# Optimization experiments

Measured on AMD Instinct MI355X. Metric: run time of the kernel, lower is better.

## Reference

```python
import jax, jax.numpy as jnp
from jax import lax
import numpy as np

T, B, D_IN, D_H = 1024, 128, 512, 1024
W_SCALE = 0.02  # keep exp(a) in a sane range, like default small Linear init


def setup_inputs() -> dict:
    key = jax.random.key(0)
    ks = jax.random.split(key, 7)
    return {
        "x": jax.random.normal(ks[0], (T, B, D_IN), dtype=jnp.float32),
        "initial_state": jax.random.normal(ks[1], (D_H,), dtype=jnp.float32),
        "u_W": jax.random.normal(ks[2], (D_H, D_IN), dtype=jnp.float32) * W_SCALE,
        "u_b": jax.random.normal(ks[3], (D_H,), dtype=jnp.float32) * W_SCALE,
        "g_W": jax.random.normal(ks[4], (D_H, D_IN + D_H), dtype=jnp.float32) * W_SCALE,
        "g_b": jax.random.normal(ks[5], (D_H,), dtype=jnp.float32) * W_SCALE,
        "a_W": jax.random.normal(ks[6], (D_H, D_IN + D_H), dtype=jnp.float32) * W_SCALE,
    }


def reference(x, initial_state, u_W, u_b, g_W, g_b, a_W):
    # x: [T, B, D_in]; returns (hts [T, B, D_h], ht [B, D_h])
    batch = x.shape[1]
    d_h = initial_state.shape[0]
    ht0 = jnp.tanh(jnp.broadcast_to(initial_state, (batch, d_h)))
    n0 = jnp.zeros((batch, d_h), dtype=x.dtype)
    d0 = jnp.zeros((batch, d_h), dtype=x.dtype)

    def step(carry, x_step):
        n, d, ht = carry
        x_merge = jnp.concatenate([x_step, ht], axis=1)  # [B, D_in + D_h]
        u = x_step @ u_W.T + u_b
        g = x_merge @ g_W.T + g_b
        a = x_merge @ a_W.T
        z = u * jnp.tanh(g)
        ea = jnp.exp(a)
        n = n + z * ea
        d = d + ea
        ht = jnp.tanh(n / d)
        return (n, d, ht), ht

    (_, _, ht), hts = lax.scan(step, (n0, d0, ht0), x)
    return hts, ht
```

## Files before the change

### kernel.cpp

```cpp
#include <hip/hip_runtime.h>
#include <math.h>

#define T_STEPS 1024
#define NB 128
#define D_IN 512
#define D_H 1024
#define K_TOT 1536
#define N_A 3072
#define N_H 2048

typedef __bf16 bf16x8 __attribute__((ext_vector_type(8)));
typedef float f32x4 __attribute__((ext_vector_type(4)));
typedef unsigned long long u64;

__device__ __forceinline__ unsigned short f2bf(float f) {
    unsigned int u = __float_as_uint(f);
    unsigned int r = 0x7fffu + ((u >> 16) & 1u);
    return (unsigned short)((u + r) >> 16);
}
__device__ __forceinline__ float bf2f(unsigned short v) {
    return __uint_as_float(((unsigned int)v) << 16);
}
__device__ __forceinline__ float fast_tanh(float x) {
    float ax = fabsf(x);
    float e = __expf(2.0f * ax);
    float t = 1.0f - 2.0f / (e + 1.0f);
    return copysignf(t, x);
}


__global__ __launch_bounds__(256) void pack_wa(
    const float* __restrict__ uW, const float* __restrict__ gW,
    const float* __restrict__ aW, unsigned short* __restrict__ wa) {
    int i = blockIdx.x * 256 + threadIdx.x;
    if (i >= N_A * D_IN) return;
    int rr = i >> 9, k = i & 511;
    float v;
    if (rr < 1024)       v = uW[(size_t)rr * D_IN + k];
    else if (rr < 2048)  v = gW[(size_t)(rr - 1024) * K_TOT + k];
    else                 v = aW[(size_t)(rr - 2048) * K_TOT + k];
    wa[i] = f2bf(v);
}

__global__ __launch_bounds__(256) void pack_wh(
    const float* __restrict__ gW, const float* __restrict__ aW,
    unsigned short* __restrict__ wh) {
    int i = blockIdx.x * 256 + threadIdx.x;
    if (i >= N_H * D_H) return;
    int rr = i >> 10, k = i & 1023;
    int g = rr >> 5, ii = rr & 31, j = g * 16 + (ii & 15);
    const float* src = (ii < 16) ? gW : aW;
    wh[i] = f2bf(src[(size_t)j * K_TOT + D_IN + k]);
}

__global__ __launch_bounds__(256) void rwa_init(
    const float* __restrict__ init_st, float* __restrict__ nbuf,
    float* __restrict__ dbuf, unsigned short* __restrict__ hbuf,
    int* __restrict__ flags) {
    int i = blockIdx.x * 256 + threadIdx.x;
    if (i >= NB * D_H) return;
    nbuf[i] = 0.f; dbuf[i] = 0.f;
    hbuf[i] = f2bf(tanhf(init_st[i & (D_H - 1)]));
    if (i < 256) flags[i] = 0;
}


__global__ __launch_bounds__(256) void phase_a(
    const float* __restrict__ x, const unsigned short* __restrict__ wa,
    const float* __restrict__ ub, const float* __restrict__ gb,
    unsigned short* __restrict__ pre)
{
    __shared__ unsigned short As[128][72];
    __shared__ unsigned short Bs[128][72];
    const int tid = threadIdx.x;
    const int bn = blockIdx.x;
    const int bm = blockIdx.y;
    const int wave = tid >> 6, lane = tid & 63;
    const int wm = wave >> 1, wn = wave & 1;
    const int lr = lane & 15, lk = lane >> 4;

    f32x4 acc[4][4] = {};

    for (int k0 = 0; k0 < D_IN; k0 += 64) {
        for (int i = tid; i < 128 * 16; i += 256) {
            int r = i >> 4, c4 = (i & 15) * 4;
            float4 v = *(const float4*)&x[(size_t)(bm * 128 + r) * D_IN + k0 + c4];
            unsigned short* d = &As[r][c4];
            d[0] = f2bf(v.x); d[1] = f2bf(v.y); d[2] = f2bf(v.z); d[3] = f2bf(v.w);
        }
        for (int i = tid; i < 128 * 8; i += 256) {
            int r = i >> 3, c8 = (i & 7) * 8;
            *(uint4*)&Bs[r][c8] =
                *(const uint4*)&wa[(size_t)(bn * 128 + r) * D_IN + k0 + c8];
        }
        __syncthreads();
        #pragma unroll
        for (int ks = 0; ks < 2; ++ks) {
            bf16x8 af[4], bfr[4];
            #pragma unroll
            for (int mf = 0; mf < 4; ++mf)
                af[mf] = *(const bf16x8*)&As[wm * 64 + mf * 16 + lr][ks * 32 + lk * 8];
            #pragma unroll
            for (int nf = 0; nf < 4; ++nf)
                bfr[nf] = *(const bf16x8*)&Bs[wn * 64 + nf * 16 + lr][ks * 32 + lk * 8];
            #pragma unroll
            for (int mf = 0; mf < 4; ++mf)
                #pragma unroll
                for (int nf = 0; nf < 4; ++nf)
                    acc[mf][nf] = __builtin_amdgcn_mfma_f32_16x16x32_bf16(
                        af[mf], bfr[nf], acc[mf][nf], 0, 0, 0);
        }
        __syncthreads();
    }

    #pragma unroll
    for (int nf = 0; nf < 4; ++nf) {
        int n = bn * 128 + wn * 64 + nf * 16 + lr;
        float bias = (n < 1024) ? ub[n] : ((n < 2048) ? gb[n - 1024] : 0.f);
        #pragma unroll
        for (int mf = 0; mf < 4; ++mf) {
            int mbase = bm * 128 + wm * 64 + mf * 16 + lk * 4;
            #pragma unroll
            for (int r = 0; r < 4; ++r) {
                int mrow = mbase + r;
                pre[((size_t)(mrow >> 7) * N_A + n) * 128 + (mrow & 127)] =
                    f2bf(acc[mf][nf][r] + bias);
            }
        }
    }
}


__global__ __launch_bounds__(512) void rwa_persist(
    const unsigned short* __restrict__ wh,
    const unsigned short* __restrict__ pre,
    unsigned short* __restrict__ hbuf,
    float* __restrict__ nbuf, float* __restrict__ dbuf,
    float* __restrict__ out,
    int* __restrict__ flags,
    int t0, int nt)
{
    __shared__ unsigned short whs[32][1024];
    __shared__ unsigned short hs[32][1024];
    __shared__ float scr[6 * 512];

    const int tid = threadIdx.x;
    const int bid = blockIdx.x;
    const int bn = bid >> 2;
    const int bm = bid & 3;
    const int wave = tid >> 6, lane = tid & 63;
    const int wm = wave >> 2;
    const int kq = wave & 3;
    const int lr = lane & 15, lk = lane >> 4;

    for (int s = tid; s < 4096; s += 512) {
        int r = s >> 7, g = s & 127;
        uint4 v = *(const uint4*)&wh[(size_t)(bn * 32 + r) * 1024 + (size_t)g * 8];
        *(uint4*)&whs[r][(g ^ (r & 7)) * 8] = v;
    }

    const int j = bn * 16 + lr;
    const int bbase = bm * 32 + wm * 16 + lk * 4;
    float nr[4], dr[4];
    if (kq == 0) {
        #pragma unroll
        for (int r = 0; r < 4; ++r) {
            size_t idx = (size_t)(bbase + r) * D_H + j;
            nr[r] = nbuf[idx]; dr[r] = dbuf[idx];
        }
    }

    const int r0 = tid >> 7;
    const int gg = tid & 127;
    const unsigned short* hsrc0 =
        hbuf + (size_t)(bm * 32 + r0) * D_H + (size_t)gg * 8;
    const int* fp = flags + bm * 64 + lane;
    __syncthreads();

    for (int l = 0; l < nt; ++l) {
        const int t = t0 + l;

        u64 puL = 0, pgL = 0, paL = 0;
        if (kq == 0) {
            size_t pb = (size_t)l * N_A * 128;
            puL = *(const u64*)&pre[pb + ((size_t)j) * 128 + bbase];
            pgL = *(const u64*)&pre[pb + ((size_t)(1024 + j)) * 128 + bbase];
            paL = *(const u64*)&pre[pb + ((size_t)(2048 + j)) * 128 + bbase];
        }

        if (t > 0) {
            if (wave == 0) {
                for (;;) {
                    int v;
                    asm volatile("global_load_dword %0, %1, off sc0 sc1\n\t"
                                 "s_waitcnt vmcnt(0)"
                                 : "=v"(v) : "v"(fp) : "memory");
                    if (__all(v >= t)) break;
                    __builtin_amdgcn_s_sleep(1);
                }
            }
            __builtin_amdgcn_s_barrier();
        }

        {
            const unsigned short* hsrc = hsrc0 + (size_t)(t & 1) * NB * D_H;
            uint4 v0, v1, v2, v3, v4, v5, v6, v7;
            asm volatile("global_load_dwordx4 %0, %1, off sc0 sc1" : "=v"(v0) : "v"(hsrc)               : "memory");
            asm volatile("global_load_dwordx4 %0, %1, off sc0 sc1" : "=v"(v1) : "v"(hsrc + 4 * D_H)     : "memory");
            asm volatile("global_load_dwordx4 %0, %1, off sc0 sc1" : "=v"(v2) : "v"(hsrc + 8 * D_H)     : "memory");
            asm volatile("global_load_dwordx4 %0, %1, off sc0 sc1" : "=v"(v3) : "v"(hsrc + 12 * D_H)    : "memory");
            asm volatile("global_load_dwordx4 %0, %1, off sc0 sc1" : "=v"(v4) : "v"(hsrc + 16 * D_H)    : "memory");
            asm volatile("global_load_dwordx4 %0, %1, off sc0 sc1" : "=v"(v5) : "v"(hsrc + 20 * D_H)    : "memory");
            asm volatile("global_load_dwordx4 %0, %1, off sc0 sc1" : "=v"(v6) : "v"(hsrc + 24 * D_H)    : "memory");
            asm volatile("global_load_dwordx4 %0, %1, off sc0 sc1" : "=v"(v7) : "v"(hsrc + 28 * D_H)    : "memory");
            asm volatile("s_waitcnt vmcnt(0)" ::: "memory");
            *(uint4*)&hs[r0 +  0][(gg ^ r0) * 8]       = v0;
            *(uint4*)&hs[r0 +  4][(gg ^ r0 ^ 4) * 8]   = v1;
            *(uint4*)&hs[r0 +  8][(gg ^ r0) * 8]       = v2;
            *(uint4*)&hs[r0 + 12][(gg ^ r0 ^ 4) * 8]   = v3;
            *(uint4*)&hs[r0 + 16][(gg ^ r0) * 8]       = v4;
            *(uint4*)&hs[r0 + 20][(gg ^ r0 ^ 4) * 8]   = v5;
            *(uint4*)&hs[r0 + 24][(gg ^ r0) * 8]       = v6;
            *(uint4*)&hs[r0 + 28][(gg ^ r0 ^ 4) * 8]   = v7;
        }
        __syncthreads();

        f32x4 accg = {}, acca = {};
        const int ar = wm * 16 + lr;
        #pragma unroll
        for (int ks = 0; ks < 8; ++ks) {
            const int k = kq * 256 + ks * 32 + lk * 8;
            const int gidx = k >> 3;
            bf16x8 av = *(const bf16x8*)&hs[ar][(gidx ^ (ar & 7)) << 3];
            bf16x8 bg = *(const bf16x8*)&whs[lr][(gidx ^ (lr & 7)) << 3];
            bf16x8 ba = *(const bf16x8*)&whs[16 + lr][(gidx ^ (lr & 7)) << 3];
            accg = __builtin_amdgcn_mfma_f32_16x16x32_bf16(av, bg, accg, 0, 0, 0);
            acca = __builtin_amdgcn_mfma_f32_16x16x32_bf16(av, ba, acca, 0, 0, 0);
        }

        if (kq != 0) {
            int base = (wm * 3 + (kq - 1)) * 512 + lane * 4;
            *(f32x4*)&scr[base]       = accg;
            *(f32x4*)&scr[base + 256] = acca;
        }
        __syncthreads();

        if (kq == 0) {
            #pragma unroll
            for (int s = 0; s < 3; ++s) {
                int base = (wm * 3 + s) * 512 + lane * 4;
                accg += *(const f32x4*)&scr[base];
                acca += *(const f32x4*)&scr[base + 256];
            }
            unsigned short* hdst = hbuf + (size_t)((t + 1) & 1) * NB * D_H;
            float hv[4];
            #pragma unroll
            for (int r = 0; r < 4; ++r) {
                float u  = bf2f((unsigned short)(puL >> (16 * r)));
                float gx = bf2f((unsigned short)(pgL >> (16 * r)));
                float ax = bf2f((unsigned short)(paL >> (16 * r)));
                float g = gx + accg[r];
                float a = ax + acca[r];
                float ea = __expf(a);
                float z = u * fast_tanh(g);
                nr[r] += z * ea;
                dr[r] += ea;
                hv[r] = fast_tanh(nr[r] / dr[r]);
                unsigned int hb = f2bf(hv[r]);
                unsigned int ob = (unsigned int)__shfl_xor((int)hb, 1);
                if (!(lr & 1)) {
                    unsigned int packed = (hb & 0xffffu) | (ob << 16);
                    unsigned short* hp = hdst + (size_t)(bbase + r) * D_H + j;
                    asm volatile("global_store_dword %0, %1, off sc0 sc1"
                                 :: "v"(hp), "v"(packed) : "memory");
                }
            }
            asm volatile("s_waitcnt vmcnt(0)" ::: "memory");

            __builtin_amdgcn_s_barrier();
            if (tid == 0) {
                int done = t + 1;
                asm volatile("global_store_dword %0, %1, off sc0 sc1"
                             :: "v"(flags + bm * 64 + bn), "v"(done) : "memory");
            }
            #pragma unroll
            for (int r = 0; r < 4; ++r) {
                size_t idx = (size_t)(bbase + r) * D_H + j;
                out[(size_t)t * NB * D_H + idx] = hv[r];
                if (t == T_STEPS - 1) out[(size_t)T_STEPS * NB * D_H + idx] = hv[r];
            }
        } else {
            __builtin_amdgcn_s_barrier();
        }
    }

    if (kq == 0) {
        #pragma unroll
        for (int r = 0; r < 4; ++r) {
            size_t idx = (size_t)(bbase + r) * D_H + j;
            nbuf[idx] = nr[r]; dbuf[idx] = dr[r];
        }
    }
}


extern "C" void kernel_launch(void* const* d_in, const int* in_sizes, int n_in,
                              void* d_out, int out_size, void* d_ws, size_t ws_size,
                              hipStream_t stream) {
    const float* x       = (const float*)d_in[0];
    const float* init_st = (const float*)d_in[1];
    const float* uW      = (const float*)d_in[2];
    const float* ub      = (const float*)d_in[3];
    const float* gW      = (const float*)d_in[4];
    const float* gb      = (const float*)d_in[5];
    const float* aW      = (const float*)d_in[6];
    float* out = (float*)d_out;

    char* ws = (char*)d_ws;
    float* nbuf = (float*)ws;                                   ws += (size_t)NB * D_H * 4;
    float* dbuf = (float*)ws;                                   ws += (size_t)NB * D_H * 4;
    unsigned short* hbuf = (unsigned short*)ws;                 ws += (size_t)2 * NB * D_H * 2;
    int* flags = (int*)ws;                                      ws += 256 * 4;
    unsigned short* wa = (unsigned short*)ws;                   ws += (size_t)N_A * D_IN * 2;
    unsigned short* wh = (unsigned short*)ws;                   ws += (size_t)N_H * D_H * 2;
    unsigned short* pre = (unsigned short*)ws;
    size_t fixed = (size_t)(ws - (char*)d_ws);
    size_t per_ct = (size_t)128 * N_A * 2;

    int CT = 1024;
    while (CT > 1 && fixed + (size_t)CT * per_ct > ws_size) CT >>= 1;

    pack_wa<<<(N_A * D_IN + 255) / 256, 256, 0, stream>>>(uW, gW, aW, wa);
    pack_wh<<<(N_H * D_H + 255) / 256, 256, 0, stream>>>(gW, aW, wh);
    rwa_init<<<(NB * D_H + 255) / 256, 256, 0, stream>>>(init_st, nbuf, dbuf, hbuf, flags);

    for (int c = 0; c < T_STEPS / CT; ++c) {
        phase_a<<<dim3(24, CT), 256, 0, stream>>>(
            x + (size_t)c * CT * NB * D_IN, wa, ub, gb, pre);
        rwa_persist<<<256, 512, 0, stream>>>(
            wh, pre, hbuf, nbuf, dbuf, out, flags, c * CT, CT);
    }
}
```

Before: 6.065 ms.

## Keep recurrent weights in registers and load h directly as MFMA operands

The persistent recurrent kernel now holds its recurrent weight slices in VGPRs instead of LDS. Each wave loads its slice of h straight from global memory as MFMA A-operands, which removes the per-step LDS staging of h and one block barrier. The tiling changes to 8 batch groups by 32 columns per block, and flags become finer-grained per 16-column half, so each wave polls only the producer flags it needs. Partial sums are reduced through a double-buffered LDS scratch with a single barrier per step, and a padding array keeps occupancy at one block per CU. The risks are higher register pressure and more flag-polling traffic from every wave.

```diff
diff --git a/kernel.cpp b/kernel.cpp
--- a/kernel.cpp
+++ b/kernel.cpp
@@ -26,6 +26,9 @@
     float e = __expf(2.0f * ax);
     float t = 1.0f - 2.0f / (e + 1.0f);
     return copysignf(t, x);
+}
+__device__ __forceinline__ bf16x8 cvt8(uint4 v) {
+    union { uint4 u; bf16x8 b; } c; c.u = v; return c.b;
 }
 
 
@@ -61,7 +64,7 @@
     if (i >= NB * D_H) return;
     nbuf[i] = 0.f; dbuf[i] = 0.f;
     hbuf[i] = f2bf(tanhf(init_st[i & (D_H - 1)]));
-    if (i < 256) flags[i] = 0;
+    if (i < 512) flags[i] = 0;
 }
 
 
@@ -131,7 +134,7 @@
 }
 
 
-__global__ __launch_bounds__(512) void rwa_persist(
+__global__ __launch_bounds__(512, 1) void rwa_persist(
     const unsigned short* __restrict__ wh,
     const unsigned short* __restrict__ pre,
     unsigned short* __restrict__ hbuf,
@@ -140,127 +143,141 @@
     int* __restrict__ flags,
     int t0, int nt)
 {
-    __shared__ unsigned short whs[32][1024];
-    __shared__ unsigned short hs[32][1024];
-    __shared__ float scr[6 * 512];
+    __shared__ float scr[2][4][7][256];
+    __shared__ char pad[28672];
 
     const int tid = threadIdx.x;
     const int bid = blockIdx.x;
-    const int bn = bid >> 2;
-    const int bm = bid & 3;
-    const int wave = tid >> 6, lane = tid & 63;
-    const int wm = wave >> 2;
-    const int kq = wave & 3;
+    const int bn = bid >> 3;
+    const int bm = bid & 7;
+    const int wave = tid >> 6;
+    const int lane = tid & 63;
     const int lr = lane & 15, lk = lane >> 4;
-
-    for (int s = tid; s < 4096; s += 512) {
-        int r = s >> 7, g = s & 127;
-        uint4 v = *(const uint4*)&wh[(size_t)(bn * 32 + r) * 1024 + (size_t)g * 8];
-        *(uint4*)&whs[r][(g ^ (r & 7)) * 8] = v;
-    }
-
-    const int j = bn * 16 + lr;
-    const int bbase = bm * 32 + wm * 16 + lk * 4;
+    const int kq = wave;
+
+    if (t0 == -1) pad[tid] = 0;
+
+    bf16x8 bg0[4], ba0[4], bg1[4], ba1[4];
+    {
+        const int kb = kq * 128 + lk * 8;
+        const unsigned short* w0 = wh + (size_t)((bn * 2 + 0) * 32 + lr) * 1024 + kb;
+        const unsigned short* w1 = wh + (size_t)((bn * 2 + 1) * 32 + lr) * 1024 + kb;
+        #pragma unroll
+        for (int ks = 0; ks < 4; ++ks) {
+            bg0[ks] = *(const bf16x8*)(w0 + ks * 32);
+            ba0[ks] = *(const bf16x8*)(w0 + 16 * 1024 + ks * 32);
+            bg1[ks] = *(const bf16x8*)(w1 + ks * 32);
+            ba1[ks] = *(const bf16x8*)(w1 + 16 * 1024 + ks * 32);
+        }
+    }
+
+    const int jh = wave;
+    const int j  = bn * 32 + jh * 16 + lr;
+    const int bb = bm * 16 + lk * 4;
     float nr[4], dr[4];
-    if (kq == 0) {
+    if (wave < 2) {
         #pragma unroll
         for (int r = 0; r < 4; ++r) {
-            size_t idx = (size_t)(bbase + r) * D_H + j;
+            size_t idx = (size_t)(bb + r) * D_H + j;
             nr[r] = nbuf[idx]; dr[r] = dbuf[idx];
         }
     }
 
-    const int r0 = tid >> 7;
-    const int gg = tid & 127;
-    const unsigned short* hsrc0 =
-        hbuf + (size_t)(bm * 32 + r0) * D_H + (size_t)gg * 8;
-    const int* fp = flags + bm * 64 + lane;
-    __syncthreads();
+    const unsigned short* abase0 =
+        hbuf + (size_t)(bm * 16 + lr) * D_H + kq * 128 + lk * 8;
+    const int pbn = kq * 4 + ((lane & 7) >> 1);
+    const int* fp = flags + bm * 64 + pbn * 2 + (lane & 1);
 
     for (int l = 0; l < nt; ++l) {
         const int t = t0 + l;
+        const int p = l & 1;
 
         u64 puL = 0, pgL = 0, paL = 0;
-        if (kq == 0) {
-            size_t pb = (size_t)l * N_A * 128;
-            puL = *(const u64*)&pre[pb + ((size_t)j) * 128 + bbase];
-            pgL = *(const u64*)&pre[pb + ((size_t)(1024 + j)) * 128 + bbase];
-            paL = *(const u64*)&pre[pb + ((size_t)(2048 + j)) * 128 + bbase];
+        if (wave < 2) {
+            const unsigned short* pp = pre + (size_t)l * (N_A * 128);
+            puL = *(const u64*)(pp + (size_t)j * 128 + bb);
+            pgL = *(const u64*)(pp + (size_t)(1024 + j) * 128 + bb);
+            paL = *(const u64*)(pp + (size_t)(2048 + j) * 128 + bb);
         }
 
         if (t > 0) {
-            if (wave == 0) {
-                for (;;) {
-                    int v;
-                    asm volatile("global_load_dword %0, %1, off sc0 sc1\n\t"
-                                 "s_waitcnt vmcnt(0)"
-                                 : "=v"(v) : "v"(fp) : "memory");
-                    if (__all(v >= t)) break;
-                    __builtin_amdgcn_s_sleep(1);
-                }
-            }
-            __builtin_amdgcn_s_barrier();
-        }
-
+            for (;;) {
+                int v;
+                asm volatile("global_load_dword %0, %1, off sc0 sc1\n\t"
+                             "s_waitcnt vmcnt(0)"
+                             : "=v"(v) : "v"(fp) : "memory");
+                if (__all(v >= t)) break;
+                __builtin_amdgcn_s_sleep(1);
+            }
+        }
+
+        const unsigned short* asrc = abase0 + (size_t)(t & 1) * (NB * D_H);
+        uint4 a0, a1, a2, a3;
+        asm volatile("global_load_dwordx4 %0, %1, off sc0 sc1"            : "=v"(a0) : "v"(asrc) : "memory");
+        asm volatile("global_load_dwordx4 %0, %1, off offset:64 sc0 sc1"  : "=v"(a1) : "v"(asrc) : "memory");
+        asm volatile("global_load_dwordx4 %0, %1, off offset:128 sc0 sc1" : "=v"(a2) : "v"(asrc) : "memory");
+        asm volatile("global_load_dwordx4 %0, %1, off offset:192 sc0 sc1" : "=v"(a3) : "v"(asrc) : "memory");
+        asm volatile("s_waitcnt vmcnt(0)" ::: "memory");
+        __builtin_amdgcn_sched_barrier(0);
+
+        f32x4 ag0 = {}, aa0 = {}, ag1 = {}, aa1 = {};
         {
-            const unsigned short* hsrc = hsrc0 + (size_t)(t & 1) * NB * D_H;
-            uint4 v0, v1, v2, v3, v4, v5, v6, v7;
-            asm volatile("global_load_dwordx4 %0, %1, off sc0 sc1" : "=v"(v0) : "v"(hsrc)               : "memory");
-            asm volatile("global_load_dwordx4 %0, %1, off sc0 sc1" : "=v"(v1) : "v"(hsrc + 4 * D_H)     : "memory");
-            asm volatile("global_load_dwordx4 %0, %1, off sc0 sc1" : "=v"(v2) : "v"(hsrc + 8 * D_H)     : "memory");
-            asm volatile("global_load_dwordx4 %0, %1, off sc0 sc1" : "=v"(v3) : "v"(hsrc + 12 * D_H)    : "memory");
-            asm volatile("global_load_dwordx4 %0, %1, off sc0 sc1" : "=v"(v4) : "v"(hsrc + 16 * D_H)    : "memory");
-            asm volatile("global_load_dwordx4 %0, %1, off sc0 sc1" : "=v"(v5) : "v"(hsrc + 20 * D_H)    : "memory");
-            asm volatile("global_load_dwordx4 %0, %1, off sc0 sc1" : "=v"(v6) : "v"(hsrc + 24 * D_H)    : "memory");
-            asm volatile("global_load_dwordx4 %0, %1, off sc0 sc1" : "=v"(v7) : "v"(hsrc + 28 * D_H)    : "memory");
-            asm volatile("s_waitcnt vmcnt(0)" ::: "memory");
-            *(uint4*)&hs[r0 +  0][(gg ^ r0) * 8]       = v0;
-            *(uint4*)&hs[r0 +  4][(gg ^ r0 ^ 4) * 8]   = v1;
-            *(uint4*)&hs[r0 +  8][(gg ^ r0) * 8]       = v2;
-            *(uint4*)&hs[r0 + 12][(gg ^ r0 ^ 4) * 8]   = v3;
-            *(uint4*)&hs[r0 + 16][(gg ^ r0) * 8]       = v4;
-            *(uint4*)&hs[r0 + 20][(gg ^ r0 ^ 4) * 8]   = v5;
-            *(uint4*)&hs[r0 + 24][(gg ^ r0) * 8]       = v6;
-            *(uint4*)&hs[r0 + 28][(gg ^ r0 ^ 4) * 8]   = v7;
+            bf16x8 av;
+            av = cvt8(a0);
+            ag0 = __builtin_amdgcn_mfma_f32_16x16x32_bf16(av, bg0[0], ag0, 0, 0, 0);
+            aa0 = __builtin_amdgcn_mfma_f32_16x16x32_bf16(av, ba0[0], aa0, 0, 0, 0);
+            ag1 = __builtin_amdgcn_mfma_f32_16x16x32_bf16(av, bg1[0], ag1, 0, 0, 0);
+            aa1 = __builtin_amdgcn_mfma_f32_16x16x32_bf16(av, ba1[0], aa1, 0, 0, 0);
+            av = cvt8(a1);
+            ag0 = __builtin_amdgcn_mfma_f32_16x16x32_bf16(av, bg0[1], ag0, 0, 0, 0);
+            aa0 = __builtin_amdgcn_mfma_f32_16x16x32_bf16(av, ba0[1], aa0, 0, 0, 0);
+            ag1 = __builtin_amdgcn_mfma_f32_16x16x32_bf16(av, bg1[1], ag1, 0, 0, 0);
+            aa1 = __builtin_amdgcn_mfma_f32_16x16x32_bf16(av, ba1[1], aa1, 0, 0, 0);
+            av = cvt8(a2);
+            ag0 = __builtin_amdgcn_mfma_f32_16x16x32_bf16(av, bg0[2], ag0, 0, 0, 0);
+            aa0 = __builtin_amdgcn_mfma_f32_16x16x32_bf16(av, ba0[2], aa0, 0, 0, 0);
+            ag1 = __builtin_amdgcn_mfma_f32_16x16x32_bf16(av, bg1[2], ag1, 0, 0, 0);
+            aa1 = __builtin_amdgcn_mfma_f32_16x16x32_bf16(av, ba1[2], aa1, 0, 0, 0);
+            av = cvt8(a3);
+            ag0 = __builtin_amdgcn_mfma_f32_16x16x32_bf16(av, bg0[3], ag0, 0, 0, 0);
+            aa0 = __builtin_amdgcn_mfma_f32_16x16x32_bf16(av, ba0[3], aa0, 0, 0, 0);
+            ag1 = __builtin_amdgcn_mfma_f32_16x16x32_bf16(av, bg1[3], ag1, 0, 0, 0);
+            aa1 = __builtin_amdgcn_mfma_f32_16x16x32_bf16(av, ba1[3], aa1, 0, 0, 0);
+        }
+
+        if (wave == 0) {
+            *(f32x4*)&scr[p][2][0][lane * 4] = ag1;
+            *(f32x4*)&scr[p][3][0][lane * 4] = aa1;
+        } else if (wave == 1) {
+            *(f32x4*)&scr[p][0][0][lane * 4] = ag0;
+            *(f32x4*)&scr[p][1][0][lane * 4] = aa0;
+        } else {
+            const int s = wave - 1;
+            *(f32x4*)&scr[p][0][s][lane * 4] = ag0;
+            *(f32x4*)&scr[p][1][s][lane * 4] = aa0;
+            *(f32x4*)&scr[p][2][s][lane * 4] = ag1;
+            *(f32x4*)&scr[p][3][s][lane * 4] = aa1;
         }
         __syncthreads();
 
-        f32x4 accg = {}, acca = {};
-        const int ar = wm * 16 + lr;
-        #pragma unroll
-        for (int ks = 0; ks < 8; ++ks) {
-            const int k = kq * 256 + ks * 32 + lk * 8;
-            const int gidx = k >> 3;
-            bf16x8 av = *(const bf16x8*)&hs[ar][(gidx ^ (ar & 7)) << 3];
-            bf16x8 bg = *(const bf16x8*)&whs[lr][(gidx ^ (lr & 7)) << 3];
-            bf16x8 ba = *(const bf16x8*)&whs[16 + lr][(gidx ^ (lr & 7)) << 3];
-            accg = __builtin_amdgcn_mfma_f32_16x16x32_bf16(av, bg, accg, 0, 0, 0);
-            acca = __builtin_amdgcn_mfma_f32_16x16x32_bf16(av, ba, acca, 0, 0, 0);
-        }
-
-        if (kq != 0) {
-            int base = (wm * 3 + (kq - 1)) * 512 + lane * 4;
-            *(f32x4*)&scr[base]       = accg;
-            *(f32x4*)&scr[base + 256] = acca;
-        }
-        __syncthreads();
-
-        if (kq == 0) {
-            #pragma unroll
-            for (int s = 0; s < 3; ++s) {
-                int base = (wm * 3 + s) * 512 + lane * 4;
-                accg += *(const f32x4*)&scr[base];
-                acca += *(const f32x4*)&scr[base + 256];
-            }
-            unsigned short* hdst = hbuf + (size_t)((t + 1) & 1) * NB * D_H;
+        if (wave < 2) {
+            f32x4 sg = (jh == 0) ? ag0 : ag1;
+            f32x4 sa = (jh == 0) ? aa0 : aa1;
+            #pragma unroll
+            for (int s = 0; s < 7; ++s) {
+                sg += *(const f32x4*)&scr[p][jh * 2 + 0][s][lane * 4];
+                sa += *(const f32x4*)&scr[p][jh * 2 + 1][s][lane * 4];
+            }
+
+            unsigned short* hdst = hbuf + (size_t)((t + 1) & 1) * (NB * D_H);
             float hv[4];
             #pragma unroll
             for (int r = 0; r < 4; ++r) {
                 float u  = bf2f((unsigned short)(puL >> (16 * r)));
                 float gx = bf2f((unsigned short)(pgL >> (16 * r)));
                 float ax = bf2f((unsigned short)(paL >> (16 * r)));
-                float g = gx + accg[r];
-                float a = ax + acca[r];
+                float g = gx + sg[r];
+                float a = ax + sa[r];
                 float ea = __expf(a);
                 float z = u * fast_tanh(g);
                 nr[r] += z * ea;
@@ -270,34 +287,31 @@
                 unsigned int ob = (unsigned int)__shfl_xor((int)hb, 1);
                 if (!(lr & 1)) {
                     unsigned int packed = (hb & 0xffffu) | (ob << 16);
-                    unsigned short* hp = hdst + (size_t)(bbase + r) * D_H + j;
+                    unsigned short* hp = hdst + (size_t)(bb + r) * D_H + j;
                     asm volatile("global_store_dword %0, %1, off sc0 sc1"
                                  :: "v"(hp), "v"(packed) : "memory");
                 }
             }
             asm volatile("s_waitcnt vmcnt(0)" ::: "memory");
-
-            __builtin_amdgcn_s_barrier();
-            if (tid == 0) {
+            if (lane == 0) {
                 int done = t + 1;
                 asm volatile("global_store_dword %0, %1, off sc0 sc1"
-                             :: "v"(flags + bm * 64 + bn), "v"(done) : "memory");
+                             :: "v"(flags + bm * 64 + bn * 2 + jh), "v"(done)
+                             : "memory");
             }
             #pragma unroll
             for (int r = 0; r < 4; ++r) {
-                size_t idx = (size_t)(bbase + r) * D_H + j;
-                out[(size_t)t * NB * D_H + idx] = hv[r];
-                if (t == T_STEPS - 1) out[(size_t)T_STEPS * NB * D_H + idx] = hv[r];
-            }
-        } else {
-            __builtin_amdgcn_s_barrier();
-        }
-    }
-
-    if (kq == 0) {
+                size_t idx = (size_t)(bb + r) * D_H + j;
+                out[(size_t)t * (NB * D_H) + idx] = hv[r];
+                if (t == T_STEPS - 1) out[(size_t)T_STEPS * (NB * D_H) + idx] = hv[r];
+            }
+        }
+    }
+
+    if (wave < 2) {
         #pragma unroll
         for (int r = 0; r < 4; ++r) {
-            size_t idx = (size_t)(bbase + r) * D_H + j;
+            size_t idx = (size_t)(bb + r) * D_H + j;
             nbuf[idx] = nr[r]; dbuf[idx] = dr[r];
         }
     }
@@ -320,7 +334,7 @@
     float* nbuf = (float*)ws;                                   ws += (size_t)NB * D_H * 4;
     float* dbuf = (float*)ws;                                   ws += (size_t)NB * D_H * 4;
     unsigned short* hbuf = (unsigned short*)ws;                 ws += (size_t)2 * NB * D_H * 2;
-    int* flags = (int*)ws;                                      ws += 256 * 4;
+    int* flags = (int*)ws;                                      ws += 512 * 4;
     unsigned short* wa = (unsigned short*)ws;                   ws += (size_t)N_A * D_IN * 2;
     unsigned short* wh = (unsigned short*)ws;                   ws += (size_t)N_H * D_H * 2;
     unsigned short* pre = (unsigned short*)ws;
```

Result: slower. 10.70 ms (+76.5%).
